# Performance work log

Hardware: AMD Instinct MI355X
Metric: run time of the kernel (lower is better)

## Reference

```python
import jax, jax.numpy as jnp
import numpy as np

I = 2048   # input_size
H = 2048   # hidden_size
O = 1024   # output_size (decode steps AND out-linear width)
LEAK = 0.01  # nn.LeakyReLU default negative_slope


def setup_inputs() -> dict:
    key = jax.random.key(0)
    ks = jax.random.split(key, 13)
    w = lambda k, shape: (jax.random.normal(k, shape, dtype=jnp.float32) * 0.02)
    return {
        "a": jax.random.normal(ks[0], (I,), dtype=jnp.float32),
        # encoder GRU (torch nn.GRU, num_layers=1): gates stacked [r; z; n]
        "enc_Wih": w(ks[1], (3 * H, I)),
        "enc_Whh": w(ks[2], (3 * H, H)),
        "enc_bih": w(ks[3], (3 * H,)),
        "enc_bhh": w(ks[4], (3 * H,)),
        # decoder into: Linear(1 -> H)
        "into_W": w(ks[5], (H, 1)),
        "into_b": w(ks[6], (H,)),
        # decoder GRU
        "dec_Wih": w(ks[7], (3 * H, H)),
        "dec_Whh": w(ks[8], (3 * H, H)),
        "dec_bih": w(ks[9], (3 * H,)),
        "dec_bhh": w(ks[10], (3 * H,)),
        # decoder out: Linear(H -> O)
        "out_W": w(ks[11], (O, H)),
        "out_b": w(ks[12], (O,)),
    }


def _gru_cell(x, h, Wih, Whh, bih, bhh):
    # torch GRU cell: gates ordered [reset; update; new]
    n_h = h.shape[0]
    gx = Wih @ x + bih          # (3H,)
    gh = Whh @ h + bhh          # (3H,)
    r = jax.nn.sigmoid(gx[:n_h] + gh[:n_h])
    z = jax.nn.sigmoid(gx[n_h:2 * n_h] + gh[n_h:2 * n_h])
    n = jnp.tanh(gx[2 * n_h:] + r * gh[2 * n_h:])
    return (1.0 - z) * n + z * h


def reference(a, enc_Wih, enc_Whh, enc_bih, enc_bhh,
              into_W, into_b, dec_Wih, dec_Whh, dec_bih, dec_bhh,
              out_W, out_b):
    n_h = enc_Whh.shape[1]
    n_out = out_W.shape[0]
    # encoder: seq_len=1, batch=1, h0=0 -> single GRU step on the flat input
    h = _gru_cell(a, jnp.zeros((n_h,), a.dtype), enc_Wih, enc_Whh, enc_bih, enc_bhh)

    def step(carry, _):
        h, x = carry                         # h: (H,), x: scalar fed-back topv
        v = into_W[:, 0] * x + into_b        # Linear(1->H) on scalar input
        v = jnp.where(v > 0, v, LEAK * v)    # LeakyReLU
        h = _gru_cell(v, h, dec_Wih, dec_Whh, dec_bih, dec_bhh)
        logits = out_W @ h + out_b           # (O,)
        topv = jnp.max(jax.nn.log_softmax(logits))  # topk(1) value
        return (h, topv), topv

    # torch.empty is uninitialized; use 0.0 as the initial decoder input
    (_, _), outs = jax.lax.scan(step, (h, jnp.zeros((), a.dtype)), None, length=n_out)
    return outs  # (output_size,) sequence of top log-prob values
```

## Files before the change

### kernel.cpp

```cpp
#include <hip/hip_runtime.h>

#define Hs 2048
#define Os 1024
#define NB 256
#define NT 512
#define BSTR 32

typedef unsigned int       uint32;
typedef unsigned long long uint64;
typedef unsigned short     ushort_t;
typedef _Float16 half2v __attribute__((ext_vector_type(2)));

__device__ __forceinline__ ushort_t f2h(float f) {
    _Float16 h = (_Float16)f;
    return __builtin_bit_cast(ushort_t, h);
}

__device__ __forceinline__ uint32 pkh2(float lo, float hi) {
#if __has_builtin(__builtin_amdgcn_cvt_pkrtz)
    return __builtin_bit_cast(uint32, __builtin_amdgcn_cvt_pkrtz(lo, hi));
#else
    return (uint32)f2h(lo) | ((uint32)f2h(hi) << 16);
#endif
}

__device__ __forceinline__ float dot2(uint32 wp, uint32 vp, float acc) {
#if __has_builtin(__builtin_amdgcn_fdot2)
    return __builtin_amdgcn_fdot2(__builtin_bit_cast(half2v, wp),
                                  __builtin_bit_cast(half2v, vp), acc, false);
#else
    half2v a = __builtin_bit_cast(half2v, wp), b = __builtin_bit_cast(half2v, vp);
    acc = fmaf((float)a.x, (float)b.x, acc);
    return fmaf((float)a.y, (float)b.y, acc);
#endif
}

__device__ __forceinline__ float dot8(uint4 wq, uint4 vq, float acc) {
    acc = dot2(wq.x, vq.x, acc); acc = dot2(wq.y, vq.y, acc);
    acc = dot2(wq.z, vq.z, acc); acc = dot2(wq.w, vq.w, acc);
    return acc;
}

__device__ __forceinline__ float dot4f(float4 w, float4 v, float acc) {
    acc = fmaf(w.x, v.x, acc); acc = fmaf(w.y, v.y, acc);
    acc = fmaf(w.z, v.z, acc); acc = fmaf(w.w, v.w, acc);
    return acc;
}

__device__ __forceinline__ int sj(int j) { return j ^ (((j >> 5) & 1) << 2); }

#define KEEP4(u) asm volatile("" : "+v"((u).x), "+v"((u).y), "+v"((u).z), "+v"((u).w))

__device__ __forceinline__ uint32 gload(const uint32* p) {
    return __hip_atomic_load(p, __ATOMIC_RELAXED, __HIP_MEMORY_SCOPE_AGENT);
}
__device__ __forceinline__ void gstore(uint32* p, uint32 v) {
    __hip_atomic_store(p, v, __ATOMIC_RELAXED, __HIP_MEMORY_SCOPE_AGENT);
}
__device__ __forceinline__ uint64 gload64(const uint64* p) {
    return __hip_atomic_load(p, __ATOMIC_RELAXED, __HIP_MEMORY_SCOPE_AGENT);
}
__device__ __forceinline__ void gstore64(uint64* p, uint64 v) {
    __hip_atomic_store(p, v, __ATOMIC_RELAXED, __HIP_MEMORY_SCOPE_AGENT);
}
__device__ __forceinline__ uint64 pack_fe(float f, uint32 ep) {
    return (uint64)__float_as_uint(f) | ((uint64)ep << 32);
}
__device__ __forceinline__ float  pk_val(uint64 v) { return __uint_as_float((uint32)v); }
__device__ __forceinline__ uint32 pk_ep(uint64 v)  { return (uint32)(v >> 32); }

__device__ __forceinline__ uint64 spin_load(const uint64* p, uint32 target) {
    uint64 v = gload64(p);
    while (pk_ep(v) < target) { __builtin_amdgcn_s_sleep(0); v = gload64(p); }
    return v;
}

__global__ void cvt_kernel(const float* __restrict__ src, ushort_t* __restrict__ dst, int n4) {
    int stride = gridDim.x * blockDim.x;
    for (int idx = blockIdx.x * blockDim.x + threadIdx.x; idx < n4; idx += stride) {
        float4 f = ((const float4*)src)[idx];
        ushort4 o;
        o.x = f2h(f.x); o.y = f2h(f.y); o.z = f2h(f.z); o.w = f2h(f.w);
        ((ushort4*)dst)[idx] = o;
    }
}

__global__ void __launch_bounds__(NT) decode_kernel(
    const float* __restrict__ a,
    const float* __restrict__ encWih,
    const float* __restrict__ encBih,
    const float* __restrict__ encBhh,
    const float* __restrict__ intoW,
    const float* __restrict__ intoB,
    const float* __restrict__ decBih,
    const float* __restrict__ decBhh,
    const float* __restrict__ outB,
    const ushort_t* __restrict__ Wih,
    const ushort_t* __restrict__ Whh,
    const ushort_t* __restrict__ Wout,
    uint64* __restrict__ hpk,
    uint64* __restrict__ pm,
    uint64* __restrict__ ps,
    uint32* __restrict__ go,
    float* __restrict__ out)
{
    const int tid  = threadIdx.x;
    const int b    = blockIdx.x;
    const int lane = tid & 63;
    const int w    = tid >> 6;
    const int i    = b * 8 + w;

    __shared__ __align__(16) float  h_enc[Hs];
    __shared__ __align__(16) uint32 h16[Hs / 2];
    __shared__ __align__(16) uint32 v16[Hs / 2];
    __shared__ float red_a[8];
    __shared__ float h_sh[8];
    __shared__ float xshare;

    const float bxr = decBih[i], bxz = decBih[i + Hs], bxn = decBih[i + 2 * Hs];
    const float bhr = decBhh[i], bhz = decBhh[i + Hs], bhn = decBhh[i + 2 * Hs];
    const float4 iw4 = ((const float4*)intoW)[tid];
    const float4 ib4 = ((const float4*)intoB)[tid];
    const float ob0 = outB[b * 4 + 0], ob1 = outB[b * 4 + 1], ob2 = outB[b * 4 + 2], ob3 = outB[b * 4 + 3];

    const ushort_t* Xr = Wih + (size_t)i * Hs;
    const ushort_t* Xz = Wih + (size_t)(i + Hs) * Hs;
    const ushort_t* Xn = Wih + (size_t)(i + 2 * Hs) * Hs;
    const ushort_t* Hr = Whh + (size_t)i * Hs;
    const ushort_t* Hz = Whh + (size_t)(i + Hs) * Hs;
    const ushort_t* Hn = Whh + (size_t)(i + 2 * Hs) * Hs;

    float hold;

    for (int k = tid; k < Hs; k += NT) h_enc[sj(k)] = a[k];
    __syncthreads();
    {
        float sr = 0.f, sz = 0.f, sn = 0.f;
        const float* Rr = encWih + (size_t)i * Hs;
        const float* Rz = encWih + (size_t)(i + Hs) * Hs;
        const float* Rn = encWih + (size_t)(i + 2 * Hs) * Hs;
#pragma unroll
        for (int it = 0; it < 4; ++it) {
            int j0 = it * 512 + lane * 8;
            float4 a0 = *(const float4*)(h_enc + sj(j0));
            float4 a1 = *(const float4*)(h_enc + sj(j0 + 4));
            sr = dot4f(*(const float4*)(Rr + j0), a0, sr);
            sr = dot4f(*(const float4*)(Rr + j0 + 4), a1, sr);
            sz = dot4f(*(const float4*)(Rz + j0), a0, sz);
            sz = dot4f(*(const float4*)(Rz + j0 + 4), a1, sz);
            sn = dot4f(*(const float4*)(Rn + j0), a0, sn);
            sn = dot4f(*(const float4*)(Rn + j0 + 4), a1, sn);
        }
#pragma unroll
        for (int m = 1; m < 64; m <<= 1) {
            sr += __shfl_xor(sr, m, 64);
            sz += __shfl_xor(sz, m, 64);
            sn += __shfl_xor(sn, m, 64);
        }
        float gxr = sr + encBih[i];
        float gxz = sz + encBih[i + Hs];
        float gxn = sn + encBih[i + 2 * Hs];
        float r = 1.f / (1.f + __expf(-(gxr + encBhh[i])));
        float z = 1.f / (1.f + __expf(-(gxz + encBhh[i + Hs])));
        float n = tanhf(gxn + r * encBhh[i + 2 * Hs]);
        hold = (1.f - z) * n;
        if (lane == 0) h_sh[w] = hold;
    }

    uint4 wXr[4], wXz[4], wXn[4], wHr[4], wHz[4], wHn[4], wO[2];
    {
        const ushort_t* R = Wout + (size_t)(b * 4 + (w >> 1)) * Hs + (w & 1) * 1024;
#pragma unroll
        for (int it = 0; it < 4; ++it) {
            int j0 = it * 512 + lane * 8;
            wXr[it] = *(const uint4*)(Xr + j0);
            wXz[it] = *(const uint4*)(Xz + j0);
            wXn[it] = *(const uint4*)(Xn + j0);
            wHr[it] = *(const uint4*)(Hr + j0);
            wHz[it] = *(const uint4*)(Hz + j0);
            wHn[it] = *(const uint4*)(Hn + j0);
        }
#pragma unroll
        for (int it = 0; it < 2; ++it)
            wO[it] = *(const uint4*)(R + it * 512 + lane * 8);
    }

    __syncthreads();
    if (tid < 4) {
        uint32 pr = pkh2(h_sh[2 * tid], h_sh[2 * tid + 1]);
        gstore64(hpk + b * 4 + tid, (uint64)pr | (1ull << 32));
    }

    {
        if (b == 0) {
            if (tid < 64) {
                uint64 va[16];
#pragma unroll
                for (int k = 0; k < 16; ++k) va[k] = gload64(hpk + tid + k * 64);
#pragma unroll
                for (int k = 0; k < 16; ++k)
                    while (pk_ep(va[k]) < 1u) { __builtin_amdgcn_s_sleep(0); va[k] = gload64(hpk + tid + k * 64); }
                if (tid < 8) gstore(go + tid * BSTR, 1u);
            }
            __syncthreads();
        } else {
            if (tid == 0) {
                const uint32* g = go + (b & 7) * BSTR;
                while (gload(g) < 1u) __builtin_amdgcn_s_sleep(0);
            }
            __syncthreads();
        }
    }
    {
        uint64 p0 = gload64(hpk + tid);
        uint64 p1 = gload64(hpk + tid + 512);
        h16[tid]       = (uint32)p0;
        h16[tid + 512] = (uint32)p1;
    }
    __syncthreads();

    for (int t = 0; t < Os; ++t) {
        const uint32 eph = (uint32)t + 2u;

        KEEP4(wXr[0]); KEEP4(wXr[1]); KEEP4(wXr[2]); KEEP4(wXr[3]);
        KEEP4(wXz[0]); KEEP4(wXz[1]); KEEP4(wXz[2]); KEEP4(wXz[3]);
        KEEP4(wXn[0]); KEEP4(wXn[1]); KEEP4(wXn[2]); KEEP4(wXn[3]);
        KEEP4(wHr[0]); KEEP4(wHr[1]); KEEP4(wHr[2]); KEEP4(wHr[3]);
        KEEP4(wHz[0]); KEEP4(wHz[1]); KEEP4(wHz[2]); KEEP4(wHz[3]);
        KEEP4(wHn[0]); KEEP4(wHn[1]); KEEP4(wHn[2]); KEEP4(wHn[3]);
        KEEP4(wO[0]);  KEEP4(wO[1]);

        float ahr = 0.f, ahz = 0.f, ahn = 0.f;
#pragma unroll
        for (int it = 0; it < 4; ++it) {
            const uint4 hq = *(const uint4*)(h16 + it * 256 + lane * 4);
            ahr = dot8(wHr[it], hq, ahr);
            ahz = dot8(wHz[it], hq, ahz);
            ahn = dot8(wHn[it], hq, ahn);
        }
#pragma unroll
        for (int m = 1; m < 64; m <<= 1) {
            ahr += __shfl_xor(ahr, m, 64);
            ahz += __shfl_xor(ahz, m, 64);
            ahn += __shfl_xor(ahn, m, 64);
        }

        if (w == 0) {
            if (t > 0) {
                const uint32 tg = (uint32)t;
                const uint64 *q0 = pm + lane,       *q1 = pm + lane + 64,
                             *q2 = pm + lane + 128, *q3 = pm + lane + 192;
                const uint64 *r0 = ps + lane,       *r1 = ps + lane + 64,
                             *r2 = ps + lane + 128, *r3 = ps + lane + 192;
                uint64 vm0 = gload64(q0), vm1 = gload64(q1), vm2 = gload64(q2), vm3 = gload64(q3);
                uint64 vs0 = gload64(r0), vs1 = gload64(r1), vs2 = gload64(r2), vs3 = gload64(r3);
                while (pk_ep(vm0) < tg) { __builtin_amdgcn_s_sleep(0); vm0 = gload64(q0); }
                while (pk_ep(vm1) < tg) { __builtin_amdgcn_s_sleep(0); vm1 = gload64(q1); }
                while (pk_ep(vm2) < tg) { __builtin_amdgcn_s_sleep(0); vm2 = gload64(q2); }
                while (pk_ep(vm3) < tg) { __builtin_amdgcn_s_sleep(0); vm3 = gload64(q3); }
                while (pk_ep(vs0) < tg) { __builtin_amdgcn_s_sleep(0); vs0 = gload64(r0); }
                while (pk_ep(vs1) < tg) { __builtin_amdgcn_s_sleep(0); vs1 = gload64(r1); }
                while (pk_ep(vs2) < tg) { __builtin_amdgcn_s_sleep(0); vs2 = gload64(r2); }
                while (pk_ep(vs3) < tg) { __builtin_amdgcn_s_sleep(0); vs3 = gload64(r3); }
                float xm = pk_val(vm0), xs = pk_val(vs0);
                {
                    float mo = pk_val(vm1), so = pk_val(vs1);
                    float M = fmaxf(xm, mo);
                    xs = xs * __expf(xm - M) + so * __expf(mo - M); xm = M;
                }
                {
                    float mo = pk_val(vm2), so = pk_val(vs2);
                    float M = fmaxf(xm, mo);
                    xs = xs * __expf(xm - M) + so * __expf(mo - M); xm = M;
                }
                {
                    float mo = pk_val(vm3), so = pk_val(vs3);
                    float M = fmaxf(xm, mo);
                    xs = xs * __expf(xm - M) + so * __expf(mo - M); xm = M;
                }
#pragma unroll
                for (int k = 1; k < 64; k <<= 1) {
                    float mo = __shfl_xor(xm, k, 64);
                    float so = __shfl_xor(xs, k, 64);
                    float M = fmaxf(xm, mo);
                    xs = xs * __expf(xm - M) + so * __expf(mo - M);
                    xm = M;
                }
                if (lane == 0) {
                    float xv = -__logf(xs);
                    xshare = xv;
                    if (b == 0) out[t - 1] = xv;
                }
            } else if (lane == 0) {
                xshare = 0.f;
            }
        }
        __syncthreads();
        const float x = xshare;

        {
            float v0 = fmaf(iw4.x, x, ib4.x); v0 = (v0 > 0.f) ? v0 : 0.01f * v0;
            float v1 = fmaf(iw4.y, x, ib4.y); v1 = (v1 > 0.f) ? v1 : 0.01f * v1;
            float v2 = fmaf(iw4.z, x, ib4.z); v2 = (v2 > 0.f) ? v2 : 0.01f * v2;
            float v3 = fmaf(iw4.w, x, ib4.w); v3 = (v3 > 0.f) ? v3 : 0.01f * v3;
            v16[2 * tid]     = pkh2(v0, v1);
            v16[2 * tid + 1] = pkh2(v2, v3);
        }
        __syncthreads();

        {
            float axr = 0.f, axz = 0.f, axn = 0.f;
#pragma unroll
            for (int it = 0; it < 4; ++it) {
                const uint4 vq = *(const uint4*)(v16 + it * 256 + lane * 4);
                axr = dot8(wXr[it], vq, axr);
                axz = dot8(wXz[it], vq, axz);
                axn = dot8(wXn[it], vq, axn);
            }
#pragma unroll
            for (int m = 1; m < 64; m <<= 1) {
                axr += __shfl_xor(axr, m, 64);
                axz += __shfl_xor(axz, m, 64);
                axn += __shfl_xor(axn, m, 64);
            }
            float r = 1.f / (1.f + __expf(-(axr + bxr + ahr + bhr)));
            float z = 1.f / (1.f + __expf(-(axz + bxz + ahz + bhz)));
            float n = tanhf(axn + bxn + r * (ahn + bhn));
            float hn = (1.f - z) * n + z * hold;
            hold = hn;
            if (lane == 0) h_sh[w] = hn;
        }
        __syncthreads();

        if (tid < 4) {
            uint32 pr = pkh2(h_sh[2 * tid], h_sh[2 * tid + 1]);
            gstore64(hpk + b * 4 + tid, (uint64)pr | ((uint64)eph << 32));
        }

        if (b == 0) {
            if (tid < 64) {
                uint64 va[16];
#pragma unroll
                for (int k = 0; k < 16; ++k) va[k] = gload64(hpk + tid + k * 64);
#pragma unroll
                for (int k = 0; k < 16; ++k)
                    while (pk_ep(va[k]) < eph) { __builtin_amdgcn_s_sleep(0); va[k] = gload64(hpk + tid + k * 64); }
                if (tid < 8) gstore(go + tid * BSTR, eph);
            }
            __syncthreads();
        } else {
            if (tid == 0) {
                const uint32* g = go + (b & 7) * BSTR;
                while (gload(g) < eph) __builtin_amdgcn_s_sleep(0);
            }
            __syncthreads();
        }

        {
            uint64 p0 = gload64(hpk + tid);
            uint64 p1 = gload64(hpk + tid + 512);
            h16[tid]       = (uint32)p0;
            h16[tid + 512] = (uint32)p1;
        }
        __syncthreads();

        {
            const int jbp = (w & 1) * 512;
            float acc = 0.f;
#pragma unroll
            for (int it = 0; it < 2; ++it) {
                const uint4 hq = *(const uint4*)(h16 + jbp + it * 256 + lane * 4);
                acc = dot8(wO[it], hq, acc);
            }
#pragma unroll
            for (int m = 1; m < 64; m <<= 1) acc += __shfl_xor(acc, m, 64);
            if (lane == 0) red_a[w] = acc;
            __syncthreads();
            if (tid == 0) {
                float l0 = red_a[0] + red_a[1] + ob0;
                float l1 = red_a[2] + red_a[3] + ob1;
                float l2 = red_a[4] + red_a[5] + ob2;
                float l3 = red_a[6] + red_a[7] + ob3;
                float m = fmaxf(fmaxf(l0, l1), fmaxf(l2, l3));
                float s = __expf(l0 - m) + __expf(l1 - m) + __expf(l2 - m) + __expf(l3 - m);
                gstore64(pm + b, pack_fe(m, (uint32)(t + 1)));
                gstore64(ps + b, pack_fe(s, (uint32)(t + 1)));
            }
        }
    }

    if (b == 0 && w == 0) {
        float xm = -1e30f, xs = 0.f;
#pragma unroll
        for (int q = 0; q < 4; ++q) {
            int p = lane + q * 64;
            uint64 vm = spin_load(pm + p, (uint32)Os);
            uint64 vs = spin_load(ps + p, (uint32)Os);
            float mo = pk_val(vm), so = pk_val(vs);
            float M = fmaxf(xm, mo);
            xs = xs * __expf(xm - M) + so * __expf(mo - M);
            xm = M;
        }
#pragma unroll
        for (int k = 1; k < 64; k <<= 1) {
            float mo = __shfl_xor(xm, k, 64);
            float so = __shfl_xor(xs, k, 64);
            float M = fmaxf(xm, mo);
            xs = xs * __expf(xm - M) + so * __expf(mo - M);
            xm = M;
        }
        if (lane == 0) out[Os - 1] = -__logf(xs);
    }
}

extern "C" void kernel_launch(void* const* d_in, const int* in_sizes, int n_in,
                              void* d_out, int out_size, void* d_ws, size_t ws_size,
                              hipStream_t stream) {
    const float* a      = (const float*)d_in[0];
    const float* encWih = (const float*)d_in[1];
    const float* encBih = (const float*)d_in[3];
    const float* encBhh = (const float*)d_in[4];
    const float* intoW  = (const float*)d_in[5];
    const float* intoB  = (const float*)d_in[6];
    const float* decWih = (const float*)d_in[7];
    const float* decWhh = (const float*)d_in[8];
    const float* decBih = (const float*)d_in[9];
    const float* decBhh = (const float*)d_in[10];
    const float* outW   = (const float*)d_in[11];
    const float* outB   = (const float*)d_in[12];

    ushort_t* wsWih  = (ushort_t*)d_ws;
    ushort_t* wsWhh  = wsWih + (size_t)3 * Hs * Hs;
    ushort_t* wsWout = wsWhh + (size_t)3 * Hs * Hs;
    uint64*   hpk    = (uint64*)(wsWout + (size_t)Os * Hs);
    uint64*   pmw    = hpk + Hs / 2;
    uint64*   psw    = pmw + NB;
    uint32*   gow    = (uint32*)(psw + NB);
    float*    out    = (float*)d_out;

    cvt_kernel<<<4096, 256, 0, stream>>>(decWih, wsWih, 3 * Hs * Hs / 4);
    cvt_kernel<<<4096, 256, 0, stream>>>(decWhh, wsWhh, 3 * Hs * Hs / 4);
    cvt_kernel<<<1024, 256, 0, stream>>>(outW,  wsWout, Os * Hs / 4);
    hipMemsetAsync(hpk, 0, (Hs / 2 + 2 * NB) * sizeof(uint64) + 8 * BSTR * sizeof(uint32), stream);

    void* args[] = {
        (void*)&a, (void*)&encWih, (void*)&encBih, (void*)&encBhh,
        (void*)&intoW, (void*)&intoB, (void*)&decBih, (void*)&decBhh,
        (void*)&outB, (void*)&wsWih, (void*)&wsWhh, (void*)&wsWout,
        (void*)&hpk, (void*)&pmw, (void*)&psw, (void*)&gow, (void*)&out
    };
    hipLaunchCooperativeKernel(reinterpret_cast<void*>(decode_kernel),
                               dim3(NB), dim3(NT), args, 0, stream);
}
```

Baseline: 5.433 ms.

## Pack softmax max and sum into one flag word and prefetch hidden state before barrier

Softmax partial max (fp32), sum (fp16) and a 16-bit epoch are now packed into a single 64-bit word, halving the per-block polls and stores in the cross-block logsumexp exchange. Non-root blocks also issue their hidden-state loads before waiting on the go flag, reload only if the epoch is stale, and block 0 fills shared memory straight from the values it already polled. This cuts memory round trips on the serial per-step critical path. The cost is fp16 precision on the softmax partial sums and a 16-bit epoch field.

```diff
diff --git a/kernel.cpp b/kernel.cpp
--- a/kernel.cpp
+++ b/kernel.cpp
@@ -63,15 +63,20 @@
 __device__ __forceinline__ void gstore64(uint64* p, uint64 v) {
     __hip_atomic_store(p, v, __ATOMIC_RELAXED, __HIP_MEMORY_SCOPE_AGENT);
 }
-__device__ __forceinline__ uint64 pack_fe(float f, uint32 ep) {
-    return (uint64)__float_as_uint(f) | ((uint64)ep << 32);
-}
-__device__ __forceinline__ float  pk_val(uint64 v) { return __uint_as_float((uint32)v); }
 __device__ __forceinline__ uint32 pk_ep(uint64 v)  { return (uint32)(v >> 32); }
 
-__device__ __forceinline__ uint64 spin_load(const uint64* p, uint32 target) {
+__device__ __forceinline__ uint64 pack_ms(float m, float s, uint32 ep) {
+    return ((uint64)__float_as_uint(m) << 32) | ((uint64)f2h(s) << 16) | (uint64)(ep & 0xffffu);
+}
+__device__ __forceinline__ uint32 ms_ep(uint64 v) { return (uint32)(v & 0xffffu); }
+__device__ __forceinline__ float  ms_m(uint64 v)  { return __uint_as_float((uint32)(v >> 32)); }
+__device__ __forceinline__ float  ms_s(uint64 v)  {
+    ushort_t b = (ushort_t)(v >> 16);
+    return (float)__builtin_bit_cast(_Float16, b);
+}
+__device__ __forceinline__ uint64 spin_ms(const uint64* p, uint32 target) {
     uint64 v = gload64(p);
-    while (pk_ep(v) < target) { __builtin_amdgcn_s_sleep(0); v = gload64(p); }
+    while (ms_ep(v) < target) { __builtin_amdgcn_s_sleep(0); v = gload64(p); }
     return v;
 }
 
@@ -100,7 +105,6 @@
     const ushort_t* __restrict__ Wout,
     uint64* __restrict__ hpk,
     uint64* __restrict__ pm,
-    uint64* __restrict__ ps,
     uint32* __restrict__ go,
     float* __restrict__ out)
 {
@@ -190,34 +194,33 @@
         uint32 pr = pkh2(h_sh[2 * tid], h_sh[2 * tid + 1]);
         gstore64(hpk + b * 4 + tid, (uint64)pr | (1ull << 32));
     }
-
-    {
-        if (b == 0) {
-            if (tid < 64) {
-                uint64 va[16];
-#pragma unroll
-                for (int k = 0; k < 16; ++k) va[k] = gload64(hpk + tid + k * 64);
-#pragma unroll
-                for (int k = 0; k < 16; ++k)
-                    while (pk_ep(va[k]) < 1u) { __builtin_amdgcn_s_sleep(0); va[k] = gload64(hpk + tid + k * 64); }
-                if (tid < 8) gstore(go + tid * BSTR, 1u);
-            }
-            __syncthreads();
-        } else {
-            if (tid == 0) {
-                const uint32* g = go + (b & 7) * BSTR;
-                while (gload(g) < 1u) __builtin_amdgcn_s_sleep(0);
-            }
-            __syncthreads();
-        }
-    }
-    {
-        uint64 p0 = gload64(hpk + tid);
-        uint64 p1 = gload64(hpk + tid + 512);
-        h16[tid]       = (uint32)p0;
-        h16[tid + 512] = (uint32)p1;
-    }
-    __syncthreads();
+    if (b == 0) {
+        if (tid < 64) {
+            uint64 va[16];
+#pragma unroll
+            for (int k = 0; k < 16; ++k) va[k] = gload64(hpk + tid + k * 64);
+#pragma unroll
+            for (int k = 0; k < 16; ++k)
+                while (pk_ep(va[k]) < 1u) { __builtin_amdgcn_s_sleep(0); va[k] = gload64(hpk + tid + k * 64); }
+            if (tid < 8) gstore(go + tid * BSTR, 1u);
+#pragma unroll
+            for (int k = 0; k < 16; ++k) h16[tid + k * 64] = (uint32)va[k];
+        }
+        __syncthreads();
+    } else {
+        uint64 sp0 = gload64(hpk + tid);
+        uint64 sp1 = gload64(hpk + tid + 512);
+        if (tid == 0) {
+            const uint32* g = go + (b & 7) * BSTR;
+            while (gload(g) < 1u) __builtin_amdgcn_s_sleep(0);
+        }
+        __syncthreads();
+        if (pk_ep(sp0) < 1u) sp0 = gload64(hpk + tid);
+        if (pk_ep(sp1) < 1u) sp1 = gload64(hpk + tid + 512);
+        h16[tid]       = (uint32)sp0;
+        h16[tid + 512] = (uint32)sp1;
+        __syncthreads();
+    }
 
     for (int t = 0; t < Os; ++t) {
         const uint32 eph = (uint32)t + 2u;
@@ -250,31 +253,24 @@
                 const uint32 tg = (uint32)t;
                 const uint64 *q0 = pm + lane,       *q1 = pm + lane + 64,
                              *q2 = pm + lane + 128, *q3 = pm + lane + 192;
-                const uint64 *r0 = ps + lane,       *r1 = ps + lane + 64,
-                             *r2 = ps + lane + 128, *r3 = ps + lane + 192;
-                uint64 vm0 = gload64(q0), vm1 = gload64(q1), vm2 = gload64(q2), vm3 = gload64(q3);
-                uint64 vs0 = gload64(r0), vs1 = gload64(r1), vs2 = gload64(r2), vs3 = gload64(r3);
-                while (pk_ep(vm0) < tg) { __builtin_amdgcn_s_sleep(0); vm0 = gload64(q0); }
-                while (pk_ep(vm1) < tg) { __builtin_amdgcn_s_sleep(0); vm1 = gload64(q1); }
-                while (pk_ep(vm2) < tg) { __builtin_amdgcn_s_sleep(0); vm2 = gload64(q2); }
-                while (pk_ep(vm3) < tg) { __builtin_amdgcn_s_sleep(0); vm3 = gload64(q3); }
-                while (pk_ep(vs0) < tg) { __builtin_amdgcn_s_sleep(0); vs0 = gload64(r0); }
-                while (pk_ep(vs1) < tg) { __builtin_amdgcn_s_sleep(0); vs1 = gload64(r1); }
-                while (pk_ep(vs2) < tg) { __builtin_amdgcn_s_sleep(0); vs2 = gload64(r2); }
-                while (pk_ep(vs3) < tg) { __builtin_amdgcn_s_sleep(0); vs3 = gload64(r3); }
-                float xm = pk_val(vm0), xs = pk_val(vs0);
+                uint64 v0 = gload64(q0), v1 = gload64(q1), v2 = gload64(q2), v3 = gload64(q3);
+                while (ms_ep(v0) < tg) { __builtin_amdgcn_s_sleep(0); v0 = gload64(q0); }
+                while (ms_ep(v1) < tg) { __builtin_amdgcn_s_sleep(0); v1 = gload64(q1); }
+                while (ms_ep(v2) < tg) { __builtin_amdgcn_s_sleep(0); v2 = gload64(q2); }
+                while (ms_ep(v3) < tg) { __builtin_amdgcn_s_sleep(0); v3 = gload64(q3); }
+                float xm = ms_m(v0), xs = ms_s(v0);
                 {
-                    float mo = pk_val(vm1), so = pk_val(vs1);
+                    float mo = ms_m(v1), so = ms_s(v1);
                     float M = fmaxf(xm, mo);
                     xs = xs * __expf(xm - M) + so * __expf(mo - M); xm = M;
                 }
                 {
-                    float mo = pk_val(vm2), so = pk_val(vs2);
+                    float mo = ms_m(v2), so = ms_s(v2);
                     float M = fmaxf(xm, mo);
                     xs = xs * __expf(xm - M) + so * __expf(mo - M); xm = M;
                 }
                 {
-                    float mo = pk_val(vm3), so = pk_val(vs3);
+                    float mo = ms_m(v3), so = ms_s(v3);
                     float M = fmaxf(xm, mo);
                     xs = xs * __expf(xm - M) + so * __expf(mo - M); xm = M;
                 }
@@ -346,23 +342,24 @@
                 for (int k = 0; k < 16; ++k)
                     while (pk_ep(va[k]) < eph) { __builtin_amdgcn_s_sleep(0); va[k] = gload64(hpk + tid + k * 64); }
                 if (tid < 8) gstore(go + tid * BSTR, eph);
+#pragma unroll
+                for (int k = 0; k < 16; ++k) h16[tid + k * 64] = (uint32)va[k];
             }
             __syncthreads();
         } else {
+            uint64 sp0 = gload64(hpk + tid);
+            uint64 sp1 = gload64(hpk + tid + 512);
             if (tid == 0) {
                 const uint32* g = go + (b & 7) * BSTR;
                 while (gload(g) < eph) __builtin_amdgcn_s_sleep(0);
             }
             __syncthreads();
-        }
-
-        {
-            uint64 p0 = gload64(hpk + tid);
-            uint64 p1 = gload64(hpk + tid + 512);
-            h16[tid]       = (uint32)p0;
-            h16[tid + 512] = (uint32)p1;
-        }
-        __syncthreads();
+            if (pk_ep(sp0) < eph) sp0 = gload64(hpk + tid);
+            if (pk_ep(sp1) < eph) sp1 = gload64(hpk + tid + 512);
+            h16[tid]       = (uint32)sp0;
+            h16[tid + 512] = (uint32)sp1;
+            __syncthreads();
+        }
 
         {
             const int jbp = (w & 1) * 512;
@@ -383,8 +380,7 @@
                 float l3 = red_a[6] + red_a[7] + ob3;
                 float m = fmaxf(fmaxf(l0, l1), fmaxf(l2, l3));
                 float s = __expf(l0 - m) + __expf(l1 - m) + __expf(l2 - m) + __expf(l3 - m);
-                gstore64(pm + b, pack_fe(m, (uint32)(t + 1)));
-                gstore64(ps + b, pack_fe(s, (uint32)(t + 1)));
+                gstore64(pm + b, pack_ms(m, s, (uint32)(t + 1)));
             }
         }
     }
@@ -393,10 +389,8 @@
         float xm = -1e30f, xs = 0.f;
 #pragma unroll
         for (int q = 0; q < 4; ++q) {
-            int p = lane + q * 64;
-            uint64 vm = spin_load(pm + p, (uint32)Os);
-            uint64 vs = spin_load(ps + p, (uint32)Os);
-            float mo = pk_val(vm), so = pk_val(vs);
+            uint64 v = spin_ms(pm + lane + q * 64, (uint32)Os);
+            float mo = ms_m(v), so = ms_s(v);
             float M = fmaxf(xm, mo);
             xs = xs * __expf(xm - M) + so * __expf(mo - M);
             xm = M;
@@ -434,20 +428,19 @@
     ushort_t* wsWout = wsWhh + (size_t)3 * Hs * Hs;
     uint64*   hpk    = (uint64*)(wsWout + (size_t)Os * Hs);
     uint64*   pmw    = hpk + Hs / 2;
-    uint64*   psw    = pmw + NB;
-    uint32*   gow    = (uint32*)(psw + NB);
+    uint32*   gow    = (uint32*)(pmw + NB);
     float*    out    = (float*)d_out;
 
     cvt_kernel<<<4096, 256, 0, stream>>>(decWih, wsWih, 3 * Hs * Hs / 4);
     cvt_kernel<<<4096, 256, 0, stream>>>(decWhh, wsWhh, 3 * Hs * Hs / 4);
     cvt_kernel<<<1024, 256, 0, stream>>>(outW,  wsWout, Os * Hs / 4);
-    hipMemsetAsync(hpk, 0, (Hs / 2 + 2 * NB) * sizeof(uint64) + 8 * BSTR * sizeof(uint32), stream);
+    hipMemsetAsync(hpk, 0, (Hs / 2 + NB) * sizeof(uint64) + 8 * BSTR * sizeof(uint32), stream);
 
     void* args[] = {
         (void*)&a, (void*)&encWih, (void*)&encBih, (void*)&encBhh,
         (void*)&intoW, (void*)&intoB, (void*)&decBih, (void*)&decBhh,
         (void*)&outB, (void*)&wsWih, (void*)&wsWhh, (void*)&wsWout,
-        (void*)&hpk, (void*)&pmw, (void*)&psw, (void*)&gow, (void*)&out
+        (void*)&hpk, (void*)&pmw, (void*)&gow, (void*)&out
     };
     hipLaunchCooperativeKernel(reinterpret_cast<void*>(decode_kernel),
                                dim3(NB), dim3(NT), args, 0, stream);
```

After: 7.570 ms. 1.39x slower.
